# Kernel optimization log

Measured on AMD Instinct MI355X. Metric: run time of the kernel, lower is better.

Reference implementation:

```python
import jax, jax.numpy as jnp
import numpy as np

B, T, C, F = 2, 2048, 2048, 8192
LN_EPS = 1e-5


def setup_inputs() -> dict:
    key = jax.random.key(0)
    ks = jax.random.split(key, 24)
    rn = lambda k, s, sc=1.0: jax.random.normal(k, s, jnp.float32) * sc
    un = lambda k, s: jax.random.uniform(k, s, jnp.float32)
    inp = {}
    inp['x'] = rn(ks[0], (B, T, C))
    inp['att_shift'] = rn(ks[1], (B, C))
    # wkv_state rows: aa (num), bb (den), pp (running max exponent)
    inp['wkv_state'] = jnp.stack([jnp.zeros((B, C)), jnp.zeros((B, C)),
                                  jnp.full((B, C), -1e38)], axis=1)
    inp['ffn_shift'] = rn(ks[2], (B, C))
    inp['ln1_g'] = jnp.ones(C); inp['ln1_b'] = jnp.zeros(C)
    inp['ln2_g'] = jnp.ones(C); inp['ln2_b'] = jnp.zeros(C)
    inp['tmk'] = un(ks[3], (C,)); inp['tmv'] = un(ks[4], (C,)); inp['tmr'] = un(ks[5], (C,))
    inp['time_decay'] = rn(ks[6], (C,), 0.5)
    inp['time_first'] = rn(ks[7], (C,), 0.5)
    inp['Wk'] = rn(ks[8], (C, C), 0.02); inp['Wv'] = rn(ks[9], (C, C), 0.02)
    inp['Wr'] = rn(ks[10], (C, C), 0.02); inp['Wo'] = rn(ks[11], (C, C), 0.02)
    inp['fmk'] = un(ks[12], (C,)); inp['fmr'] = un(ks[13], (C,))
    inp['Fk'] = rn(ks[14], (C, F), 0.02)
    inp['Fr'] = rn(ks[15], (C, C), 0.02)
    inp['Fv'] = rn(ks[16], (F, C), 0.02)
    return inp


def layer_norm(x, g, b):
    m = jnp.mean(x, axis=-1, keepdims=True)
    v = jnp.mean(jnp.square(x - m), axis=-1, keepdims=True)
    return (x - m) * jax.lax.rsqrt(v + LN_EPS) * g + b


def wkv(w, u, k, v, state):
    # w: -exp(time_decay) [C], u: time_first [C]; k,v: [B,T,C]; state: [B,3,C]
    def step(carry, kv_t):
        aa, bb, pp = carry
        kt, vt = kv_t
        ww = u + kt
        p = jnp.maximum(pp, ww)
        e1 = jnp.exp(pp - p)
        e2 = jnp.exp(ww - p)
        y = (e1 * aa + e2 * vt) / (e1 * bb + e2)
        ww2 = pp + w
        p2 = jnp.maximum(ww2, kt)
        e1b = jnp.exp(ww2 - p2)
        e2b = jnp.exp(kt - p2)
        return (e1b * aa + e2b * vt, e1b * bb + e2b, p2), y
    carry0 = (state[:, 0], state[:, 1], state[:, 2])
    (aa, bb, pp), ys = jax.lax.scan(step, carry0,
                                    (k.transpose(1, 0, 2), v.transpose(1, 0, 2)))
    return ys.transpose(1, 0, 2), jnp.stack([aa, bb, pp], axis=1)


def reference(x, att_shift, wkv_state, ffn_shift, ln1_g, ln1_b, ln2_g, ln2_b,
              tmk, tmv, tmr, time_decay, time_first, Wk, Wv, Wr, Wo,
              fmk, fmr, Fk, Fr, Fv):
    # ---- time-mix (attention) ----
    x1 = layer_norm(x, ln1_g, ln1_b)
    xx = jnp.concatenate([att_shift[:, None, :], x1[:, :-1]], axis=1)
    xk = x1 * tmk + xx * (1.0 - tmk)
    xv = x1 * tmv + xx * (1.0 - tmv)
    xr = x1 * tmr + xx * (1.0 - tmr)
    k = jnp.einsum('btc,cd->btd', xk, Wk)
    v = jnp.einsum('btc,cd->btd', xv, Wv)
    r = jnp.einsum('btc,cd->btd', xr, Wr)
    y, new_wkv = wkv(-jnp.exp(time_decay), time_first, k, v, wkv_state)
    x = x + jnp.einsum('btd,dc->btc', jax.nn.sigmoid(r) * y, Wo)
    # ---- channel-mix (FFN) ----
    x2 = layer_norm(x, ln2_g, ln2_b)
    xx2 = jnp.concatenate([ffn_shift[:, None, :], x2[:, :-1]], axis=1)
    xk2 = x2 * fmk + xx2 * (1.0 - fmk)
    xr2 = x2 * fmr + xx2 * (1.0 - fmr)
    kf = jnp.square(jax.nn.relu(jnp.einsum('btc,cf->btf', xk2, Fk)))
    kv = jnp.einsum('btf,fc->btc', kf, Fv)
    x = x + jax.nn.sigmoid(jnp.einsum('btc,cd->btd', xr2, Fr)) * kv
    return x, x1[:, -1], new_wkv, x2[:, -1]
```

## Files before the change

### kernel.cpp

```cpp
#include <hip/hip_runtime.h>
#include <stdint.h>

#define B_ 2
#define T_ 2048
#define C_ 2048
#define F_ 8192
#define M_ 4096
#define BC_ 4096
#define CHB 16
#define TCH 16
#define LC2 128

typedef __attribute__((ext_vector_type(8))) __bf16 bf16x8;
typedef __attribute__((ext_vector_type(4))) float f32x4;

__device__ __forceinline__ unsigned short f2bf(float f) {
  union { float f; unsigned u; } v; v.f = f;
  unsigned r = v.u + 0x7fffu + ((v.u >> 16) & 1u);
  return (unsigned short)(r >> 16);
}
__device__ __forceinline__ float b2f(unsigned short h) {
  union { unsigned u; float f; } v; v.u = ((unsigned)h) << 16; return v.f;
}

__device__ __forceinline__ void gload16(const void* g, void* l) {
  __builtin_amdgcn_global_load_lds((__attribute__((address_space(1))) void*)g,
                                   (__attribute__((address_space(3))) void*)l,
                                   16, 0, 0);
}

__global__ __launch_bounds__(256) void k_transpose_cast(
    const float* __restrict__ W, unsigned short* __restrict__ WT, int K, int N) {
  __shared__ unsigned short tile[32][33];
  const int n0 = blockIdx.x * 32, k0 = blockIdx.y * 32;
  const int tx = threadIdx.x & 31, ty = threadIdx.x >> 5;
#pragma unroll
  for (int i = 0; i < 4; ++i)
    tile[ty + 8 * i][tx] = f2bf(W[(size_t)(k0 + ty + 8 * i) * N + n0 + tx]);
  __syncthreads();
#pragma unroll
  for (int i = 0; i < 4; ++i)
    WT[(size_t)(n0 + ty + 8 * i) * K + k0 + tx] = tile[tx][ty + 8 * i];
}

__global__ __launch_bounds__(256) void k_layernorm(
    const float* __restrict__ x, const float* __restrict__ g,
    const float* __restrict__ beta, unsigned short* __restrict__ y,
    float* __restrict__ last_out) {
  const int row = blockIdx.x;
  const int t = row & (T_ - 1);
  const int bi = row >> 11;
  const float* xr = x + (size_t)row * C_;
  const int base = threadIdx.x * 8;
  float lv[8];
  {
    float4 a = *(const float4*)(xr + base);
    float4 b = *(const float4*)(xr + base + 4);
    lv[0]=a.x; lv[1]=a.y; lv[2]=a.z; lv[3]=a.w; lv[4]=b.x; lv[5]=b.y; lv[6]=b.z; lv[7]=b.w;
  }
  float s = 0.f, q = 0.f;
#pragma unroll
  for (int j = 0; j < 8; ++j) { s += lv[j]; q += lv[j] * lv[j]; }
#pragma unroll
  for (int o = 32; o > 0; o >>= 1) { s += __shfl_down(s, o); q += __shfl_down(q, o); }
  __shared__ float rs[4], rq[4];
  if ((threadIdx.x & 63) == 0) { rs[threadIdx.x >> 6] = s; rq[threadIdx.x >> 6] = q; }
  __syncthreads();
  s = rs[0] + rs[1] + rs[2] + rs[3];
  q = rq[0] + rq[1] + rq[2] + rq[3];
  const float mean = s * (1.f / C_);
  const float var = q * (1.f / C_) - mean * mean;
  const float inv = 1.f / sqrtf(var + 1e-5f);
  float ov[8];
  unsigned short o8[8];
#pragma unroll
  for (int j = 0; j < 8; ++j) {
    ov[j] = (lv[j] - mean) * inv * g[base + j] + beta[base + j];
    o8[j] = f2bf(ov[j]);
  }
  *(uint4*)(y + (size_t)row * C_ + base) = *(uint4*)o8;
  if (last_out != nullptr && t == T_ - 1) {
    float* lp = last_out + (size_t)bi * C_ + base;
    *(float4*)lp = make_float4(ov[0], ov[1], ov[2], ov[3]);
    *(float4*)(lp + 4) = make_float4(ov[4], ov[5], ov[6], ov[7]);
  }
}

__global__ __launch_bounds__(256) void k_mix3(
    const unsigned short* __restrict__ x1, const float* __restrict__ shift,
    const float* __restrict__ tmk, const float* __restrict__ tmv,
    const float* __restrict__ tmr,
    unsigned short* __restrict__ xk, unsigned short* __restrict__ xv,
    unsigned short* __restrict__ xr) {
  const int row = blockIdx.x;
  const int t = row & (T_ - 1);
  const int bi = row >> 11;
  const int c0 = threadIdx.x * 8;
  const size_t o = (size_t)row * C_ + c0;
  unsigned short cur8[8];
  *(uint4*)cur8 = *(const uint4*)(x1 + o);
  float pv[8];
  if (t == 0) {
    const float* sp = shift + (size_t)bi * C_ + c0;
#pragma unroll
    for (int j = 0; j < 8; ++j) pv[j] = sp[j];
  } else {
    unsigned short p8[8];
    *(uint4*)p8 = *(const uint4*)(x1 + o - C_);
#pragma unroll
    for (int j = 0; j < 8; ++j) pv[j] = b2f(p8[j]);
  }
  unsigned short ok[8], ov[8], orr[8];
#pragma unroll
  for (int j = 0; j < 8; ++j) {
    const float a = b2f(cur8[j]), p = pv[j];
    const float mk = tmk[c0 + j], mv = tmv[c0 + j], mr = tmr[c0 + j];
    ok[j]  = f2bf(a * mk + p * (1.f - mk));
    ov[j]  = f2bf(a * mv + p * (1.f - mv));
    orr[j] = f2bf(a * mr + p * (1.f - mr));
  }
  *(uint4*)(xk + o) = *(uint4*)ok;
  *(uint4*)(xv + o) = *(uint4*)ov;
  *(uint4*)(xr + o) = *(uint4*)orr;
}

__global__ __launch_bounds__(256) void k_mix2(
    const unsigned short* __restrict__ x2, const float* __restrict__ shift,
    const float* __restrict__ fmk, const float* __restrict__ fmr,
    unsigned short* __restrict__ xk2, unsigned short* __restrict__ xr2) {
  const int row = blockIdx.x;
  const int t = row & (T_ - 1);
  const int bi = row >> 11;
  const int c0 = threadIdx.x * 8;
  const size_t o = (size_t)row * C_ + c0;
  unsigned short cur8[8];
  *(uint4*)cur8 = *(const uint4*)(x2 + o);
  float pv[8];
  if (t == 0) {
    const float* sp = shift + (size_t)bi * C_ + c0;
#pragma unroll
    for (int j = 0; j < 8; ++j) pv[j] = sp[j];
  } else {
    unsigned short p8[8];
    *(uint4*)p8 = *(const uint4*)(x2 + o - C_);
#pragma unroll
    for (int j = 0; j < 8; ++j) pv[j] = b2f(p8[j]);
  }
  unsigned short ok[8], orr[8];
#pragma unroll
  for (int j = 0; j < 8; ++j) {
    const float a = b2f(cur8[j]), p = pv[j];
    const float mk = fmk[c0 + j], mr = fmr[c0 + j];
    ok[j]  = f2bf(a * mk + p * (1.f - mk));
    orr[j] = f2bf(a * mr + p * (1.f - mr));
  }
  *(uint4*)(xk2 + o) = *(uint4*)ok;
  *(uint4*)(xr2 + o) = *(uint4*)orr;
}

__global__ __launch_bounds__(256) void k_wkv_blk(
    const float* __restrict__ kk, const float* __restrict__ vv,
    const float* __restrict__ td, const float* __restrict__ tf,
    const float* __restrict__ st, float* __restrict__ y,
    float* __restrict__ out_state) {
  __shared__ float sA[TCH][CHB], sB[TCH][CHB], sP[TCH][CHB];
  const int blk = blockIdx.x;
  const int bi = blk >> 7;
  const int tx = threadIdx.x & 15;
  const int ty = threadIdx.x >> 4;
  const int c = ((blk & 127) * CHB) + tx;
  const float w = -expf(td[c]);
  const float u = tf[c];
  const size_t base = (size_t)bi * T_ * C_ + (size_t)ty * LC2 * C_ + c;
  const float* kp = kk + base;
  const float* vp = vv + base;
  float aa = 0.f, bb = 0.f, pp = -1e38f;
#pragma unroll 8
  for (int i = 0; i < LC2; ++i) {
    const float kt = kp[(size_t)i * C_], vt = vp[(size_t)i * C_];
    const float ww2 = pp + w;
    const float p2 = fmaxf(ww2, kt);
    const float e1b = expf(ww2 - p2), e2b = expf(kt - p2);
    aa = e1b * aa + e2b * vt;
    bb = e1b * bb + e2b;
    pp = p2;
  }
  sA[ty][tx] = aa; sB[ty][tx] = bb; sP[ty][tx] = pp;
  __syncthreads();
  if (ty == 0) {
    const float* s0 = st + (size_t)bi * 3 * C_;
    float ca = s0[c], cb = s0[C_ + c], cp = s0[2 * C_ + c];
    const float wL = w * (float)LC2;
#pragma unroll
    for (int j = 0; j < TCH; ++j) {
      const float a2 = sA[j][tx], b2 = sB[j][tx], p2 = sP[j][tx];
      sA[j][tx] = ca; sB[j][tx] = cb; sP[j][tx] = cp;
      const float pd = cp + wL;
      const float pm = fmaxf(pd, p2);
      const float e1 = expf(pd - pm), e2 = expf(p2 - pm);
      ca = e1 * ca + e2 * a2;
      cb = e1 * cb + e2 * b2;
      cp = pm;
    }
  }
  __syncthreads();
  aa = sA[ty][tx]; bb = sB[ty][tx]; pp = sP[ty][tx];
  float* yp = y + base;
#pragma unroll 4
  for (int i = 0; i < LC2; ++i) {
    const float kt = kp[(size_t)i * C_], vt = vp[(size_t)i * C_];
    const float ww = u + kt;
    const float p = fmaxf(pp, ww);
    const float e1 = expf(pp - p), e2 = expf(ww - p);
    yp[(size_t)i * C_] = (e1 * aa + e2 * vt) / (e1 * bb + e2);
    const float ww2 = pp + w;
    const float p2 = fmaxf(ww2, kt);
    const float e1b = expf(ww2 - p2), e2b = expf(kt - p2);
    aa = e1b * aa + e2b * vt;
    bb = e1b * bb + e2b;
    pp = p2;
  }
  if (ty == TCH - 1) {
    float* ob = out_state + (size_t)bi * 3 * C_;
    ob[c] = aa; ob[C_ + c] = bb; ob[2 * C_ + c] = pp;
  }
}

__global__ __launch_bounds__(256) void k_sry(
    const unsigned short* __restrict__ r, const float* __restrict__ y,
    unsigned short* __restrict__ sry) {
  const int nv = M_ * C_ / 8;
  for (int i = blockIdx.x * 256 + threadIdx.x; i < nv; i += gridDim.x * 256) {
    unsigned short r8[8];
    *(uint4*)r8 = ((const uint4*)r)[i];
    float4 ya = ((const float4*)y)[2 * i], yb = ((const float4*)y)[2 * i + 1];
    const float yv[8] = {ya.x, ya.y, ya.z, ya.w, yb.x, yb.y, yb.z, yb.w};
    unsigned short o8[8];
#pragma unroll
    for (int j = 0; j < 8; ++j) {
      const float s = 1.f / (1.f + expf(-b2f(r8[j])));
      o8[j] = f2bf(s * yv[j]);
    }
    ((uint4*)sry)[i] = *(uint4*)o8;
  }
}

template <int EPI, int SWZ>
__global__ __launch_bounds__(512, 1) void k_gemm8(
    const unsigned short* __restrict__ A, const unsigned short* __restrict__ BT,
    int K, int Nn, void* __restrict__ out,
    const float* __restrict__ aux1, const float* __restrict__ aux2) {
  __shared__ unsigned short lds[49152];
  const int tid = threadIdx.x;
  const int lane = tid & 63;
  const int wid = tid >> 6;
  int mBase, nBase;
  if (SWZ) {
    const int gx = gridDim.x;
    int wg = blockIdx.y * gx + blockIdx.x;
    const int nwg = gx * gridDim.y;
    wg = (wg & 7) * (nwg >> 3) + (wg >> 3);
    mBase = (wg / gx) * 128;
    nBase = (wg % gx) * 256;
  } else {
    mBase = blockIdx.y * 128;
    nBase = blockIdx.x * 256;
  }
  const int wr = (wid >> 2) * 64;
  const int wc = (wid & 3) * 64;
  const int r16 = lane & 15, kq = lane >> 4;
  const int lrow = lane >> 3;
  const int lslot = (lane & 7) ^ lrow;
  const int xsw = r16 & 7;
  f32x4 acc[4][4] = {};

  const int nt = K >> 6;
#pragma unroll
  for (int j = 0; j < 2; ++j)
    gload16(A + (size_t)(mBase + j * 64 + wid * 8 + lrow) * K + lslot * 8,
            &lds[j * 4096 + wid * 512]);
#pragma unroll
  for (int j = 0; j < 4; ++j)
    gload16(BT + (size_t)(nBase + j * 64 + wid * 8 + lrow) * K + lslot * 8,
            &lds[16384 + j * 4096 + wid * 512]);
  asm volatile("s_waitcnt vmcnt(0)" ::: "memory");
  asm volatile("s_barrier" ::: "memory");

  int cur = 0;
  for (int t = 0; t < nt; ++t) {
    const int kb2 = (t + 1) << 6;
    const bool pf = (t + 1 < nt);
    const int ca = cur * 8192, cbo = 16384 + cur * 16384;
    const int na = (cur ^ 1) * 8192, nb = 16384 + (cur ^ 1) * 16384;
    bf16x8 af[2][2], bq[2][2];
#pragma unroll
    for (int qm = 0; qm < 2; ++qm) {
#pragma unroll
      for (int qn = 0; qn < 2; ++qn) {
        if (qn == 0) {
#pragma unroll
          for (int dm = 0; dm < 2; ++dm)
#pragma unroll
            for (int s = 0; s < 2; ++s)
              af[dm][s] = *(const bf16x8*)&lds[ca + (wr + (qm * 2 + dm) * 16 + r16) * 64 +
                                               (((s * 4 + kq) ^ xsw) * 8)];
        }
#pragma unroll
        for (int dn = 0; dn < 2; ++dn)
#pragma unroll
          for (int s = 0; s < 2; ++s)
            bq[dn][s] = *(const bf16x8*)&lds[cbo + (wc + (qn * 2 + dn) * 16 + r16) * 64 +
                                             (((s * 4 + kq) ^ xsw) * 8)];
        const int ph = qm * 2 + qn;
        if (pf) {
          if (ph == 0) {
            gload16(A + (size_t)(mBase + 0 + wid * 8 + lrow) * K + kb2 + lslot * 8,
                    &lds[na + 0 + wid * 512]);
            gload16(A + (size_t)(mBase + 64 + wid * 8 + lrow) * K + kb2 + lslot * 8,
                    &lds[na + 4096 + wid * 512]);
          } else if (ph == 1) {
            gload16(BT + (size_t)(nBase + 0 + wid * 8 + lrow) * K + kb2 + lslot * 8,
                    &lds[nb + 0 + wid * 512]);
            gload16(BT + (size_t)(nBase + 64 + wid * 8 + lrow) * K + kb2 + lslot * 8,
                    &lds[nb + 4096 + wid * 512]);
          } else if (ph == 2) {
            gload16(BT + (size_t)(nBase + 128 + wid * 8 + lrow) * K + kb2 + lslot * 8,
                    &lds[nb + 8192 + wid * 512]);
            gload16(BT + (size_t)(nBase + 192 + wid * 8 + lrow) * K + kb2 + lslot * 8,
                    &lds[nb + 12288 + wid * 512]);
          }
        }
        asm volatile("s_barrier" ::: "memory");
        __builtin_amdgcn_s_setprio(1);
#pragma unroll
        for (int dm = 0; dm < 2; ++dm)
#pragma unroll
          for (int dn = 0; dn < 2; ++dn)
#pragma unroll
            for (int s = 0; s < 2; ++s)
              acc[qm * 2 + dm][qn * 2 + dn] = __builtin_amdgcn_mfma_f32_16x16x32_bf16(
                  af[dm][s], bq[dn][s], acc[qm * 2 + dm][qn * 2 + dn], 0, 0, 0);
        __builtin_amdgcn_s_setprio(0);
        if (ph == 3) asm volatile("s_waitcnt vmcnt(0)" ::: "memory");
        asm volatile("s_barrier" ::: "memory");
      }
    }
    cur ^= 1;
  }

  const int c0 = kq * 4;
#pragma unroll
  for (int m = 0; m < 4; ++m) {
#pragma unroll
    for (int n = 0; n < 4; ++n) {
      const int col = nBase + wc + n * 16 + r16;
#pragma unroll
      for (int e = 0; e < 4; ++e) {
        const int rowg = mBase + wr + m * 16 + c0 + e;
        const size_t idx = (size_t)rowg * Nn + col;
        const float va = acc[m][n][e];
        if (EPI == 0) {
          ((float*)out)[idx] = va;
        } else if (EPI == 1) {
          const float t = va > 0.f ? va : 0.f;
          ((unsigned short*)out)[idx] = f2bf(t * t);
        } else if (EPI == 2) {
          ((float*)out)[idx] = aux1[idx] + va;
        } else if (EPI == 3) {
          const float s = 1.f / (1.f + expf(-va));
          ((float*)out)[idx] = aux1[idx] + s * aux2[idx];
        } else {
          ((unsigned short*)out)[idx] = f2bf(va);
        }
      }
    }
  }
}

extern "C" void kernel_launch(void* const* d_in, const int* in_sizes, int n_in,
                              void* d_out, int out_size, void* d_ws, size_t ws_size,
                              hipStream_t stream) {
  const float* x          = (const float*)d_in[0];
  const float* att_shift  = (const float*)d_in[1];
  const float* wkv_state  = (const float*)d_in[2];
  const float* ffn_shift  = (const float*)d_in[3];
  const float* ln1_g = (const float*)d_in[4];
  const float* ln1_b = (const float*)d_in[5];
  const float* ln2_g = (const float*)d_in[6];
  const float* ln2_b = (const float*)d_in[7];
  const float* tmk = (const float*)d_in[8];
  const float* tmv = (const float*)d_in[9];
  const float* tmr = (const float*)d_in[10];
  const float* time_decay = (const float*)d_in[11];
  const float* time_first = (const float*)d_in[12];
  const float* Wk = (const float*)d_in[13];
  const float* Wv = (const float*)d_in[14];
  const float* Wr = (const float*)d_in[15];
  const float* Wo = (const float*)d_in[16];
  const float* fmk = (const float*)d_in[17];
  const float* fmr = (const float*)d_in[18];
  const float* Fk = (const float*)d_in[19];
  const float* Fr = (const float*)d_in[20];
  const float* Fv = (const float*)d_in[21];

  const size_t MB = 1ull << 20;
  char* ws = (char*)d_ws;
  if (ws_size < 176 * MB) return;

  unsigned short* Wslot = (unsigned short*)(ws);
  float*          kBuf  = (float*)(ws + 32 * MB);
  float*          vBuf  = (float*)(ws + 64 * MB);
  float*          yBuf  = (float*)(ws + 96 * MB);
  unsigned short* h1    = (unsigned short*)(ws + 128 * MB);
  unsigned short* h2    = (unsigned short*)(ws + 144 * MB);
  unsigned short* h3    = (unsigned short*)(ws + 160 * MB);
  unsigned short* xrT   = (unsigned short*)kBuf;
  unsigned short* kf    = (unsigned short*)kBuf;
  float*          kv    = (float*)h1;

  float* outb    = (float*)d_out;
  float* x1_last = outb + (size_t)M_ * C_;
  float* wkv_out = x1_last + (size_t)B_ * C_;
  float* x2_last = wkv_out + (size_t)B_ * 3 * C_;

  const dim3 gCC(C_ / 32, C_ / 32);
  const dim3 gC8(C_ / 256, M_ / 128);
  const dim3 gF8(F_ / 256, M_ / 128);

  k_layernorm<<<M_, 256, 0, stream>>>(x, ln1_g, ln1_b, h1, x1_last);
  k_mix3<<<M_, 256, 0, stream>>>(h1, att_shift, tmk, tmv, tmr, h2, h3, xrT);
  k_transpose_cast<<<gCC, 256, 0, stream>>>(Wr, Wslot, C_, C_);
  k_gemm8<4,0><<<gC8, 512, 0, stream>>>(xrT, Wslot, C_, C_, h1, nullptr, nullptr);
  k_transpose_cast<<<gCC, 256, 0, stream>>>(Wk, Wslot, C_, C_);
  k_gemm8<0,0><<<gC8, 512, 0, stream>>>(h2, Wslot, C_, C_, kBuf, nullptr, nullptr);
  k_transpose_cast<<<gCC, 256, 0, stream>>>(Wv, Wslot, C_, C_);
  k_gemm8<0,0><<<gC8, 512, 0, stream>>>(h3, Wslot, C_, C_, vBuf, nullptr, nullptr);
  k_wkv_blk<<<dim3(BC_ / CHB), 256, 0, stream>>>(kBuf, vBuf, time_decay, time_first,
                                                 wkv_state, yBuf, wkv_out);
  k_sry<<<1024, 256, 0, stream>>>(h1, yBuf, h2);
  k_transpose_cast<<<gCC, 256, 0, stream>>>(Wo, Wslot, C_, C_);
  k_gemm8<2,0><<<gC8, 512, 0, stream>>>(h2, Wslot, C_, C_, yBuf, x, nullptr);

  k_layernorm<<<M_, 256, 0, stream>>>(yBuf, ln2_g, ln2_b, h1, x2_last);
  k_mix2<<<M_, 256, 0, stream>>>(h1, ffn_shift, fmk, fmr, h2, h3);
  k_transpose_cast<<<dim3(F_ / 32, C_ / 32), 256, 0, stream>>>(Fk, Wslot, C_, F_);
  k_gemm8<1,1><<<gF8, 512, 0, stream>>>(h2, Wslot, C_, F_, kf, nullptr, nullptr);
  k_transpose_cast<<<dim3(C_ / 32, F_ / 32), 256, 0, stream>>>(Fv, Wslot, F_, C_);
  k_gemm8<0,1><<<gC8, 512, 0, stream>>>(kf, Wslot, F_, C_, kv, nullptr, nullptr);
  k_transpose_cast<<<gCC, 256, 0, stream>>>(Fr, Wslot, C_, C_);
  k_gemm8<3,0><<<gC8, 512, 0, stream>>>(h3, Wslot, C_, C_, d_out, yBuf, kv);
}
```

Baseline: 758.4 us.

## Triple-buffer GEMM LDS tiles to prefetch two K-steps ahead

Changes the bf16 GEMM's shared-memory pipeline from double to triple buffering. Loads are issued two K-tiles ahead, and the per-iteration wait becomes vmcnt(6), so one tile's loads can remain in flight while another is consumed. LDS use grows from 96KB to 144KB per block. The goal is to hide more global load latency behind MFMA work, at the cost of more LDS and more complex wait counting.

```diff
diff --git a/kernel.cpp b/kernel.cpp
--- a/kernel.cpp
+++ b/kernel.cpp
@@ -250,7 +250,7 @@
     const unsigned short* __restrict__ A, const unsigned short* __restrict__ BT,
     int K, int Nn, void* __restrict__ out,
     const float* __restrict__ aux1, const float* __restrict__ aux2) {
-  __shared__ unsigned short lds[49152];
+  __shared__ unsigned short lds[73728];
   const int tid = threadIdx.x;
   const int lane = tid & 63;
   const int wid = tid >> 6;
@@ -274,24 +274,38 @@
   const int xsw = r16 & 7;
   f32x4 acc[4][4] = {};
 
+  const unsigned short* gA0 = A  + (size_t)(mBase + 0   + wid * 8 + lrow) * K + lslot * 8;
+  const unsigned short* gA1 = A  + (size_t)(mBase + 64  + wid * 8 + lrow) * K + lslot * 8;
+  const unsigned short* gB0 = BT + (size_t)(nBase + 0   + wid * 8 + lrow) * K + lslot * 8;
+  const unsigned short* gB1 = BT + (size_t)(nBase + 64  + wid * 8 + lrow) * K + lslot * 8;
+  const unsigned short* gB2 = BT + (size_t)(nBase + 128 + wid * 8 + lrow) * K + lslot * 8;
+  const unsigned short* gB3 = BT + (size_t)(nBase + 192 + wid * 8 + lrow) * K + lslot * 8;
+  const int wof = wid * 512;
+
   const int nt = K >> 6;
-#pragma unroll
-  for (int j = 0; j < 2; ++j)
-    gload16(A + (size_t)(mBase + j * 64 + wid * 8 + lrow) * K + lslot * 8,
-            &lds[j * 4096 + wid * 512]);
-#pragma unroll
-  for (int j = 0; j < 4; ++j)
-    gload16(BT + (size_t)(nBase + j * 64 + wid * 8 + lrow) * K + lslot * 8,
-            &lds[16384 + j * 4096 + wid * 512]);
-  asm volatile("s_waitcnt vmcnt(0)" ::: "memory");
+  gload16(gA0, &lds[0 + wof]);
+  gload16(gA1, &lds[4096 + wof]);
+  gload16(gB0, &lds[8192 + wof]);
+  gload16(gB1, &lds[12288 + wof]);
+  gload16(gB2, &lds[16384 + wof]);
+  gload16(gB3, &lds[20480 + wof]);
+  gload16(gA0 + 64, &lds[24576 + 0 + wof]);
+  gload16(gA1 + 64, &lds[24576 + 4096 + wof]);
+  gload16(gB0 + 64, &lds[24576 + 8192 + wof]);
+  gload16(gB1 + 64, &lds[24576 + 12288 + wof]);
+  gload16(gB2 + 64, &lds[24576 + 16384 + wof]);
+  gload16(gB3 + 64, &lds[24576 + 20480 + wof]);
+  asm volatile("s_waitcnt vmcnt(6)" ::: "memory");
   asm volatile("s_barrier" ::: "memory");
 
-  int cur = 0;
+  int cb = 0;
   for (int t = 0; t < nt; ++t) {
-    const int kb2 = (t + 1) << 6;
-    const bool pf = (t + 1 < nt);
-    const int ca = cur * 8192, cbo = 16384 + cur * 16384;
-    const int na = (cur ^ 1) * 8192, nb = 16384 + (cur ^ 1) * 16384;
+    const int nb = (cb >= 1) ? cb - 1 : 2;
+    const int ca = cb * 24576;
+    const int cbo = cb * 24576 + 8192;
+    const int nba = nb * 24576;
+    const int kb2 = (t + 2) << 6;
+    const bool pf = (t + 2) < nt;
     bf16x8 af[2][2], bq[2][2];
 #pragma unroll
     for (int qm = 0; qm < 2; ++qm) {
@@ -314,20 +328,14 @@
         const int ph = qm * 2 + qn;
         if (pf) {
           if (ph == 0) {
-            gload16(A + (size_t)(mBase + 0 + wid * 8 + lrow) * K + kb2 + lslot * 8,
-                    &lds[na + 0 + wid * 512]);
-            gload16(A + (size_t)(mBase + 64 + wid * 8 + lrow) * K + kb2 + lslot * 8,
-                    &lds[na + 4096 + wid * 512]);
+            gload16(gA0 + kb2, &lds[nba + 0 + wof]);
+            gload16(gA1 + kb2, &lds[nba + 4096 + wof]);
           } else if (ph == 1) {
-            gload16(BT + (size_t)(nBase + 0 + wid * 8 + lrow) * K + kb2 + lslot * 8,
-                    &lds[nb + 0 + wid * 512]);
-            gload16(BT + (size_t)(nBase + 64 + wid * 8 + lrow) * K + kb2 + lslot * 8,
-                    &lds[nb + 4096 + wid * 512]);
+            gload16(gB0 + kb2, &lds[nba + 8192 + wof]);
+            gload16(gB1 + kb2, &lds[nba + 12288 + wof]);
           } else if (ph == 2) {
-            gload16(BT + (size_t)(nBase + 128 + wid * 8 + lrow) * K + kb2 + lslot * 8,
-                    &lds[nb + 8192 + wid * 512]);
-            gload16(BT + (size_t)(nBase + 192 + wid * 8 + lrow) * K + kb2 + lslot * 8,
-                    &lds[nb + 12288 + wid * 512]);
+            gload16(gB2 + kb2, &lds[nba + 16384 + wof]);
+            gload16(gB3 + kb2, &lds[nba + 20480 + wof]);
           }
         }
         asm volatile("s_barrier" ::: "memory");
@@ -341,11 +349,17 @@
               acc[qm * 2 + dm][qn * 2 + dn] = __builtin_amdgcn_mfma_f32_16x16x32_bf16(
                   af[dm][s], bq[dn][s], acc[qm * 2 + dm][qn * 2 + dn], 0, 0, 0);
         __builtin_amdgcn_s_setprio(0);
-        if (ph == 3) asm volatile("s_waitcnt vmcnt(0)" ::: "memory");
+        if (ph == 3) {
+          if (pf) {
+            asm volatile("s_waitcnt vmcnt(6)" ::: "memory");
+          } else if (t + 1 < nt) {
+            asm volatile("s_waitcnt vmcnt(0)" ::: "memory");
+          }
+        }
         asm volatile("s_barrier" ::: "memory");
       }
     }
-    cur ^= 1;
+    cb = (cb == 2) ? 0 : cb + 1;
   }
 
   const int c0 = kq * 4;
```

Result: faster. 740.8 us (-2.3%).
